# Kernel tuning notes

Measured on AMD Instinct MI355X. Metric: run time of the kernel, lower is better.

The kernel has to match this reference:

```python
import jax, jax.numpy as jnp
import numpy as np

SCALE = 2  # scale_factor; r = SCALE**2 must match kernels dim 2


def setup_inputs() -> dict:
    key = jax.random.key(0)
    k1, k2 = jax.random.split(key)
    burst = jax.random.normal(k1, (4, 8, 3, 128, 128), dtype=jnp.float32)
    # per-pixel adaptive kernels: (n, d, r, k, k, h, w), r = scale^2, k = 5
    kernels = jax.random.normal(k2, (4, 8, 4, 5, 5, 128, 128), dtype=jnp.float32)
    return {"burst": burst, "kernels": kernels}


def _adaptive_conv(burst, kernels):
    # burst: (n, d, c, h, w); kernels: (n, d, r, k, k, h, w)
    n, d, c, h, w = burst.shape
    k = kernels.shape[3]
    pad = k // 2
    padded = jnp.pad(burst, ((0, 0), (0, 0), (0, 0), (pad, pad), (pad, pad)))
    # gather kxk shifted windows -> (n, d, c, k, k, h, w); loop is over fixed k*k taps
    patches = jnp.stack(
        [jnp.stack([padded[..., i:i + h, j:j + w] for j in range(k)], axis=-3)
         for i in range(k)], axis=-4)
    # weighted sum over the kxk taps; burst channel c broadcasts against kernel r
    return jnp.einsum('ndcijhw,ndrijhw->ndcrhw', patches, kernels)


def _pixel_shuffle(x, s):
    # x: (n, d, c, r=s*s, h, w) -> (n, d, c, h*s, w*s), torch PixelShuffle order
    n, d, c, r, h, w = x.shape
    x = x.reshape(n, d, c, s, s, h, w)
    x = x.transpose(0, 1, 2, 5, 3, 6, 4)  # (n, d, c, h, s_i, w, s_j)
    return x.reshape(n, d, c, h * s, w * s)


def reference(burst, kernels):
    convolved = _adaptive_conv(burst, kernels)
    return _pixel_shuffle(convolved, SCALE)
```

## Files before the change

kernel.cpp:

```cpp
#include <hip/hip_runtime.h>

#define HH 128
#define WW 128
#define CC 3
#define RR 4
#define KK 5
#define ND 32
#define HW (HH*WW)

__global__ __launch_bounds__(256) void adaptive_conv_ps(
    const float* __restrict__ burst,
    const float* __restrict__ kern,
    float* __restrict__ out)
{
    int t  = blockIdx.x * blockDim.x + threadIdx.x;
    int w  = t & (WW - 1);
    int h  = (t >> 7) & (HH - 1);
    int nd = t >> 14;

    const float* bptr = burst + (size_t)nd * CC * HW;
    const float* kptr = kern  + (size_t)nd * RR * KK * KK * HW + h * WW + w;

    float patch[CC][KK * KK];
#pragma unroll
    for (int c = 0; c < CC; ++c) {
#pragma unroll
        for (int i = 0; i < KK; ++i) {
            int  y  = h + i - 2;
            bool yv = (unsigned)y < (unsigned)HH;
#pragma unroll
            for (int j = 0; j < KK; ++j) {
                int  x = w + j - 2;
                bool v = yv && ((unsigned)x < (unsigned)WW);
                patch[c][i * KK + j] = v ? bptr[c * HW + y * WW + x] : 0.0f;
            }
        }
    }

    float acc[CC][RR];
#pragma unroll
    for (int c = 0; c < CC; ++c)
#pragma unroll
        for (int r = 0; r < RR; ++r)
            acc[c][r] = 0.0f;

#pragma unroll
    for (int r = 0; r < RR; ++r) {
#pragma unroll
        for (int ij = 0; ij < KK * KK; ++ij) {
            float kv = kptr[(size_t)(r * KK * KK + ij) * HW];
#pragma unroll
            for (int c = 0; c < CC; ++c)
                acc[c][r] += kv * patch[c][ij];
        }
    }

#pragma unroll
    for (int c = 0; c < CC; ++c) {
#pragma unroll
        for (int si = 0; si < 2; ++si) {
            float2 v = make_float2(acc[c][si * 2 + 0], acc[c][si * 2 + 1]);
            float* o = out + (((size_t)(nd * CC + c) * (2 * HH) + (2 * h + si)) * (2 * WW)) + 2 * w;
            *(float2*)o = v;
        }
    }
}

extern "C" void kernel_launch(void* const* d_in, const int* in_sizes, int n_in,
                              void* d_out, int out_size, void* d_ws, size_t ws_size,
                              hipStream_t stream) {
    const float* burst = (const float*)d_in[0];
    const float* kern  = (const float*)d_in[1];
    float* out = (float*)d_out;

    const int total = ND * HH * WW;
    const int block = 256;
    const int grid  = total / block;
    adaptive_conv_ps<<<grid, block, 0, stream>>>(burst, kern, out);
}
```

Baseline: 298.1 us.

## Stage burst rows in shared memory and compute four pixels per thread

Each block loads a 12-row padded burst tile for all channels into LDS, then each thread computes four adjacent output pixels, reading kernel weights as float4 and reusing an 8-wide row of burst values across the taps. Output is written as float4 pairs in pixel-shuffle order. This cuts redundant global burst loads and widens kernel-weight loads, but reduces the grid to 512 blocks, which lowers occupancy for a bandwidth-bound kernel.

```diff
diff --git a/kernel.cpp b/kernel.cpp
--- a/kernel.cpp
+++ b/kernel.cpp
@@ -6,52 +6,76 @@
 #define RR 4
 #define KK 5
 #define ND 32
-#define HW (HH*WW)
+#define HW (HH * WW)
 
-__global__ __launch_bounds__(256) void adaptive_conv_ps(
+#define TROWS 12
+#define TS    132
+#define TSIZE (CC * TROWS * TS)
+
+__global__ __launch_bounds__(256, 4) void adaptive_conv_ps(
     const float* __restrict__ burst,
     const float* __restrict__ kern,
     float* __restrict__ out)
 {
-    int t  = blockIdx.x * blockDim.x + threadIdx.x;
-    int w  = t & (WW - 1);
-    int h  = (t >> 7) & (HH - 1);
-    int nd = t >> 14;
+    __shared__ float tile[TSIZE];
 
-    const float* bptr = burst + (size_t)nd * CC * HW;
-    const float* kptr = kern  + (size_t)nd * RR * KK * KK * HW + h * WW + w;
+    const int tid = threadIdx.x;
+    const int nd  = blockIdx.x >> 4;
+    const int h0  = (blockIdx.x & 15) << 3;
 
-    float patch[CC][KK * KK];
-#pragma unroll
-    for (int c = 0; c < CC; ++c) {
-#pragma unroll
-        for (int i = 0; i < KK; ++i) {
-            int  y  = h + i - 2;
-            bool yv = (unsigned)y < (unsigned)HH;
-#pragma unroll
-            for (int j = 0; j < KK; ++j) {
-                int  x = w + j - 2;
-                bool v = yv && ((unsigned)x < (unsigned)WW);
-                patch[c][i * KK + j] = v ? bptr[c * HW + y * WW + x] : 0.0f;
-            }
-        }
+    const float* bbase = burst + (size_t)nd * CC * HW;
+    for (int idx = tid; idx < TSIZE; idx += 256) {
+        int c   = idx / (TROWS * TS);
+        int rem = idx - c * (TROWS * TS);
+        int row = rem / TS;
+        int col = rem - row * TS;
+        int y = h0 - 2 + row;
+        int x = col - 2;
+        float v = 0.0f;
+        if ((unsigned)y < (unsigned)HH && (unsigned)x < (unsigned)WW)
+            v = bbase[c * HW + y * WW + x];
+        tile[idx] = v;
     }
+    __syncthreads();
 
-    float acc[CC][RR];
+    const int lrow = tid >> 5;
+    const int w0   = (tid & 31) << 2;
+    const int h    = h0 + lrow;
+
+    const float* kbase = kern + (size_t)nd * RR * KK * KK * HW + h * WW + w0;
+
+    float acc[CC][RR][4];
 #pragma unroll
     for (int c = 0; c < CC; ++c)
 #pragma unroll
         for (int r = 0; r < RR; ++r)
-            acc[c][r] = 0.0f;
+#pragma unroll
+            for (int p = 0; p < 4; ++p)
+                acc[c][r][p] = 0.0f;
 
+    for (int i = 0; i < KK; ++i) {
+        float rowv[CC][8];
 #pragma unroll
-    for (int r = 0; r < RR; ++r) {
+        for (int c = 0; c < CC; ++c) {
+            const float4* rp =
+                (const float4*)&tile[c * TROWS * TS + (lrow + i) * TS + w0];
+            *(float4*)&rowv[c][0] = rp[0];
+            *(float4*)&rowv[c][4] = rp[1];
+        }
 #pragma unroll
-        for (int ij = 0; ij < KK * KK; ++ij) {
-            float kv = kptr[(size_t)(r * KK * KK + ij) * HW];
+        for (int j = 0; j < KK; ++j) {
+            float kv[RR][4];
+#pragma unroll
+            for (int r = 0; r < RR; ++r)
+                *(float4*)kv[r] =
+                    *(const float4*)(kbase + (size_t)((r * KK + i) * KK + j) * HW);
 #pragma unroll
             for (int c = 0; c < CC; ++c)
-                acc[c][r] += kv * patch[c][ij];
+#pragma unroll
+                for (int r = 0; r < RR; ++r)
+#pragma unroll
+                    for (int p = 0; p < 4; ++p)
+                        acc[c][r][p] += kv[r][p] * rowv[c][j + p];
         }
     }
 
@@ -59,9 +83,15 @@
     for (int c = 0; c < CC; ++c) {
 #pragma unroll
         for (int si = 0; si < 2; ++si) {
-            float2 v = make_float2(acc[c][si * 2 + 0], acc[c][si * 2 + 1]);
-            float* o = out + (((size_t)(nd * CC + c) * (2 * HH) + (2 * h + si)) * (2 * WW)) + 2 * w;
-            *(float2*)o = v;
+            float4 v0, v1;
+            v0.x = acc[c][si * 2 + 0][0]; v0.y = acc[c][si * 2 + 1][0];
+            v0.z = acc[c][si * 2 + 0][1]; v0.w = acc[c][si * 2 + 1][1];
+            v1.x = acc[c][si * 2 + 0][2]; v1.y = acc[c][si * 2 + 1][2];
+            v1.z = acc[c][si * 2 + 0][3]; v1.w = acc[c][si * 2 + 1][3];
+            float* o = out + (((size_t)(nd * CC + c) * (2 * HH) + (2 * h + si)) * (2 * WW))
+                           + 2 * w0;
+            ((float4*)o)[0] = v0;
+            ((float4*)o)[1] = v1;
         }
     }
 }
@@ -73,8 +103,5 @@
     const float* kern  = (const float*)d_in[1];
     float* out = (float*)d_out;
 
-    const int total = ND * HH * WW;
-    const int block = 256;
-    const int grid  = total / block;
-    adaptive_conv_ps<<<grid, block, 0, stream>>>(burst, kern, out);
+    adaptive_conv_ps<<<ND * 16, 256, 0, stream>>>(burst, kern, out);
 }
```

New measurement: 325.0 us. 9.0% more time.
